# Optimization experiments

Hardware: AMD Instinct MI355X
Metric: run time of the kernel (lower is better)

## Reference

```python
import jax, jax.numpy as jnp
import numpy as np

N, D, K, STEPS, LAYERS, E = 20000, 128, 16, 2, 2, 8192


def setup_inputs() -> dict:
    key = jax.random.key(0)
    ks = jax.random.split(key, 8)
    return {
        "edges": jax.random.randint(ks[0], (E, 2), 0, N),
        "labels": jax.random.randint(ks[1], (E,), 0, 2).astype(jnp.int32),
        "neighbors": jax.random.randint(ks[2], (STEPS, N, K), 0, N),
        "embeddings": jax.random.normal(ks[3], (N, D), jnp.float32),
        "fc_w": jax.random.normal(ks[4], (2 * D,), jnp.float32) / np.sqrt(2.0 * D),
        "fc_b": jnp.zeros((), jnp.float32),
        "layer_w": jax.random.normal(ks[5], (LAYERS, D, D), jnp.float32) / np.sqrt(float(D)),
        "layer_b": jnp.zeros((LAYERS, D), jnp.float32),
    }


def _attention_all_nodes(embeddings, neighbors, fc_w, fc_b):
    # Vectorized GAT-style per-node attention over all N nodes, summed over steps.
    d = embeddings.shape[-1]
    w_n, w_s = fc_w[:d], fc_w[d:]  # fc applied to concat([neigh, self]) splits linearly
    out = jnp.zeros_like(embeddings)
    self_score = embeddings @ w_s  # [N]
    for s in range(neighbors.shape[0]):  # small fixed step count (2)
        nb = neighbors[s]                               # [N, K]
        neigh_emb = embeddings[nb]                      # [N, K, d]
        scores = neigh_emb @ w_n + self_score[:, None] + fc_b  # [N, K]
        scores = jnp.where(scores >= 0, scores, 0.2 * scores)  # LeakyReLU(0.2)
        attn = jax.nn.softmax(scores, axis=1)                  # softmax over neighbors
        k = nb.shape[1]
        # sum_k (neigh_emb * attn + self_emb) = weighted sum + K * self_emb
        agg = jnp.einsum("nkd,nk->nd", neigh_emb, attn) + k * embeddings
        out = out + agg
    return out


def reference(edges, labels, neighbors, embeddings, fc_w, fc_b, layer_w, layer_b):
    d = embeddings.shape[-1]
    att = _attention_all_nodes(embeddings, neighbors, fc_w, fc_b)  # [N, d]
    src, dst = edges[:, 0], edges[:, 1]
    use_att = (labels == 1)[:, None]
    src_e = jnp.where(use_att, att[src], embeddings[src])  # [E, d]
    dst_e = jnp.where(use_att, att[dst], embeddings[dst])  # [E, d]
    # layers applied in PARALLEL to the same input, relu'd, then summed
    src_l = jax.nn.relu(jnp.einsum("ed,lfd->led", src_e, layer_w) + layer_b[:, None, :])
    dst_l = jax.nn.relu(jnp.einsum("ed,lfd->led", dst_e, layer_w) + layer_b[:, None, :])
    src_sum = jnp.sum(src_l, axis=0)  # [E, d]
    dst_sum = jnp.sum(dst_l, axis=0)
    diff = jnp.sum((src_sum - dst_sum) ** 2, axis=1) / d  # [E]
    predicts = jnp.exp(-diff)
    loss = 0.5 * (labels.astype(predicts.dtype) - predicts) ** 2
    return jnp.sum(loss)
```

## Files before the change

### kernel.cpp

```cpp
#include <hip/hip_runtime.h>

#define N_NODES 20000
#define D 128
#define K 16
#define STEPS 2
#define E_EDGES 8192

#define SCORE_BLOCKS 2500
#define EDGE_BLOCKS 256
#define EDGE_WAVES (EDGE_BLOCKS * 8)


__device__ __forceinline__ unsigned short f2bf(float f) {
    unsigned u = __float_as_uint(f);
    u += 0x7FFFu + ((u >> 16) & 1u);
    return (unsigned short)(u >> 16);
}
__device__ __forceinline__ float bf2f(unsigned short h) {
    return __uint_as_float(((unsigned)h) << 16);
}

__global__ __launch_bounds__(256) void pre_kernel(
    const float* __restrict__ emb, const float* __restrict__ fc_w,
    const float* __restrict__ layer_w,
    unsigned short* __restrict__ emb_h, float* __restrict__ nscore,
    float* __restrict__ sscore, float* __restrict__ wsum,
    float* __restrict__ out)
{
    const int b = blockIdx.x;
    const int t = threadIdx.x;

    if (b < SCORE_BLOCKS) {
        const int wave = (b * 256 + t) >> 6;
        const int lane = t & 63;
        const int half = lane >> 5, sub = lane & 31;
        const int node = 2 * wave + half;

        const float4 e4  = *(const float4*)(emb + (size_t)node * D + sub * 4);
        const float4 wn4 = *(const float4*)(fc_w + sub * 4);
        const float4 ws4 = *(const float4*)(fc_w + D + sub * 4);
        float dn = e4.x * wn4.x + e4.y * wn4.y + e4.z * wn4.z + e4.w * wn4.w;
        float ds = e4.x * ws4.x + e4.y * ws4.y + e4.z * ws4.z + e4.w * ws4.w;
        #pragma unroll
        for (int off = 16; off > 0; off >>= 1) {
            dn += __shfl_xor(dn, off, 64);
            ds += __shfl_xor(ds, off, 64);
        }
        if (sub == 0) { nscore[node] = dn; sscore[node] = ds; }

        ushort4 h;
        h.x = f2bf(e4.x); h.y = f2bf(e4.y); h.z = f2bf(e4.z); h.w = f2bf(e4.w);
        *(ushort4*)(emb_h + (size_t)node * D + sub * 4) = h;
    } else {
        const int l = t >> 7, d = t & 127;
        const float* p = layer_w + (size_t)l * D * D + d;
        float s = 0.f;
        #pragma unroll
        for (int f = 0; f < D; f += 16) {
            float tmp[16];
            #pragma unroll
            for (int j = 0; j < 16; ++j) tmp[j] = p[(size_t)(f + j) * D];
            #pragma unroll
            for (int j = 0; j < 16; ++j) s += tmp[j];
        }
        wsum[t] = s;
        if (t == 0) out[0] = 0.f;
    }
}

__global__ __launch_bounds__(512) void edge_kernel(
    const int* __restrict__ edges, const int* __restrict__ labels,
    const int* __restrict__ neighbors, const float* __restrict__ emb,
    const unsigned short* __restrict__ emb_h,
    const float* __restrict__ nscore, const float* __restrict__ sscore,
    const float* __restrict__ fc_b, const float* __restrict__ wsum,
    const float* __restrict__ layer_b, float* __restrict__ out)
{
    __shared__ float part[8];
    const int t = threadIdx.x;
    const int lane = t & 63, wv = t >> 6;
    const int half = lane >> 5, sub = lane & 31;
    const int gw = blockIdx.x * 8 + wv;
    const float bias = fc_b[0];

    const float4 w0 = *(const float4*)(wsum + sub * 4);
    const float4 w1 = *(const float4*)(wsum + D + sub * 4);
    const float4 b0 = *(const float4*)(layer_b + sub * 4);
    const float4 b1 = *(const float4*)(layer_b + D + sub * 4);

    float local = 0.f;
    for (int e = gw; e < E_EDGES; e += EDGE_WAVES) {
        const int lab = labels[e];
        const int node = edges[2 * e + half];

        float4 x;
        if (lab == 1) {
            const int step = sub >> 4;
            const int idx = neighbors[((size_t)step * N_NODES + node) * K + (sub & 15)];
            const float raw = nscore[idx] + sscore[node] + bias;
            float sc = (raw >= 0.f) ? raw : 0.2f * raw;

            float m = sc;
            #pragma unroll
            for (int off = 8; off > 0; off >>= 1) m = fmaxf(m, __shfl_xor(m, off, 64));
            const float ex = __expf(sc - m);
            float den = ex;
            #pragma unroll
            for (int off = 8; off > 0; off >>= 1) den += __shfl_xor(den, off, 64);
            const float a = ex / den;

            const float4 e4 = *(const float4*)(emb + (size_t)node * D + sub * 4);
            x.x = (float)(STEPS * K) * e4.x;
            x.y = (float)(STEPS * K) * e4.y;
            x.z = (float)(STEPS * K) * e4.z;
            x.w = (float)(STEPS * K) * e4.w;
            const int base_lane = half << 5;
            #pragma unroll 8
            for (int k2 = 0; k2 < 32; ++k2) {
                const int   sl   = base_lane + k2;
                const int   idxk = __shfl(idx, sl, 64);
                const float ak   = __shfl(a, sl, 64);
                const ushort4 vh = *(const ushort4*)(emb_h + (size_t)idxk * D + sub * 4);
                x.x += ak * bf2f(vh.x);
                x.y += ak * bf2f(vh.y);
                x.z += ak * bf2f(vh.z);
                x.w += ak * bf2f(vh.w);
            }
        } else {
            x = *(const float4*)(emb + (size_t)node * D + sub * 4);
        }

        float4 ss;
        ss.x = fmaxf(x.x * w0.x + b0.x, 0.f) + fmaxf(x.x * w1.x + b1.x, 0.f);
        ss.y = fmaxf(x.y * w0.y + b0.y, 0.f) + fmaxf(x.y * w1.y + b1.y, 0.f);
        ss.z = fmaxf(x.z * w0.z + b0.z, 0.f) + fmaxf(x.z * w1.z + b1.z, 0.f);
        ss.w = fmaxf(x.w * w0.w + b0.w, 0.f) + fmaxf(x.w * w1.w + b1.w, 0.f);

        const float ox = __shfl_xor(ss.x, 32, 64);
        const float oy = __shfl_xor(ss.y, 32, 64);
        const float oz = __shfl_xor(ss.z, 32, 64);
        const float ow = __shfl_xor(ss.w, 32, 64);
        const float dx = ss.x - ox, dy = ss.y - oy, dz = ss.z - oz, dw = ss.w - ow;
        float v = dx * dx + dy * dy + dz * dz + dw * dw;
        #pragma unroll
        for (int off = 16; off > 0; off >>= 1) v += __shfl_xor(v, off, 64);

        const float pred = __expf(-(v * (1.0f / (float)D)));
        const float l = (float)lab - pred;
        local += 0.5f * l * l;
    }
    if (lane == 0) part[wv] = local;
    __syncthreads();
    if (t == 0) {
        float s = 0.f;
        #pragma unroll
        for (int i = 0; i < 8; ++i) s += part[i];
        atomicAdd(out, s);
    }
}

extern "C" void kernel_launch(void* const* d_in, const int* in_sizes, int n_in,
                              void* d_out, int out_size, void* d_ws, size_t ws_size,
                              hipStream_t stream) {
    const int*   edges     = (const int*)  d_in[0];
    const int*   labels    = (const int*)  d_in[1];
    const int*   neighbors = (const int*)  d_in[2];
    const float* emb       = (const float*)d_in[3];
    const float* fc_w      = (const float*)d_in[4];
    const float* fc_b      = (const float*)d_in[5];
    const float* layer_w   = (const float*)d_in[6];
    const float* layer_b   = (const float*)d_in[7];
    float* out = (float*)d_out;

    unsigned short* emb_h = (unsigned short*)d_ws;
    float* nscore = (float*)((char*)d_ws + (size_t)N_NODES * D * 2);
    float* sscore = nscore + N_NODES;
    float* wsum   = sscore + N_NODES;

    pre_kernel<<<SCORE_BLOCKS + 1, 256, 0, stream>>>(
        emb, fc_w, layer_w, emb_h, nscore, sscore, wsum, out);

    edge_kernel<<<EDGE_BLOCKS, 512, 0, stream>>>(
        edges, labels, neighbors, emb, emb_h, nscore, sscore,
        fc_b, wsum, layer_b, out);
}
```

Measured before the change: 95.48 us.

## Fuse preprocessing and edge kernels into one persistent kernel with grid barrier

Merges the node-score/bf16-conversion pre-pass and the edge loss pass into a single 256-block kernel. The two phases are separated by a software grid barrier built on global atomic counters and a generation number. This removes one kernel launch and the gap between launches. In exchange, it relies on all 256 blocks being co-resident, and the pre-pass now runs as a grid-stride loop over fewer waves. The emb row load is also hoisted so it is issued before the label branch.

Result: slower. 110.2 us (+15.4%).

```diff
diff --git a/kernel.cpp b/kernel.cpp
--- a/kernel.cpp
+++ b/kernel.cpp
@@ -6,10 +6,13 @@
 #define STEPS 2
 #define E_EDGES 8192
 
-#define SCORE_BLOCKS 2500
-#define EDGE_BLOCKS 256
-#define EDGE_WAVES (EDGE_BLOCKS * 8)
+#define GRID_BLOCKS 256
+#define TOTAL_WAVES (GRID_BLOCKS * 8)
+#define NODE_PAIRS (N_NODES / 2)
 
+
+__device__ unsigned g_cnt = 0u;
+__device__ unsigned g_gen = 0u;
 
 __device__ __forceinline__ unsigned short f2bf(float f) {
     unsigned u = __float_as_uint(f);
@@ -20,82 +23,92 @@
     return __uint_as_float(((unsigned)h) << 16);
 }
 
-__global__ __launch_bounds__(256) void pre_kernel(
-    const float* __restrict__ emb, const float* __restrict__ fc_w,
-    const float* __restrict__ layer_w,
+__global__ __launch_bounds__(512) void fused_kernel(
+    const int* __restrict__ edges, const int* __restrict__ labels,
+    const int* __restrict__ neighbors, const float* __restrict__ emb,
+    const float* __restrict__ fc_w, const float* __restrict__ fc_b,
+    const float* __restrict__ layer_w, const float* __restrict__ layer_b,
     unsigned short* __restrict__ emb_h, float* __restrict__ nscore,
     float* __restrict__ sscore, float* __restrict__ wsum,
     float* __restrict__ out)
 {
+    __shared__ float part[8];
+    const int t = threadIdx.x;
     const int b = blockIdx.x;
-    const int t = threadIdx.x;
+    const int lane = t & 63, wv = t >> 6;
+    const int half = lane >> 5, sub = lane & 31;
+    const int gw = b * 8 + wv;
 
-    if (b < SCORE_BLOCKS) {
-        const int wave = (b * 256 + t) >> 6;
-        const int lane = t & 63;
-        const int half = lane >> 5, sub = lane & 31;
-        const int node = 2 * wave + half;
+    const unsigned g0 = __hip_atomic_load(&g_gen, __ATOMIC_RELAXED, __HIP_MEMORY_SCOPE_AGENT);
 
-        const float4 e4  = *(const float4*)(emb + (size_t)node * D + sub * 4);
+    {
         const float4 wn4 = *(const float4*)(fc_w + sub * 4);
         const float4 ws4 = *(const float4*)(fc_w + D + sub * 4);
-        float dn = e4.x * wn4.x + e4.y * wn4.y + e4.z * wn4.z + e4.w * wn4.w;
-        float ds = e4.x * ws4.x + e4.y * ws4.y + e4.z * ws4.z + e4.w * ws4.w;
-        #pragma unroll
-        for (int off = 16; off > 0; off >>= 1) {
-            dn += __shfl_xor(dn, off, 64);
-            ds += __shfl_xor(ds, off, 64);
+        for (int p = gw; p < NODE_PAIRS; p += TOTAL_WAVES) {
+            const int node = 2 * p + half;
+            const float4 e4 = *(const float4*)(emb + (size_t)node * D + sub * 4);
+            float dn = e4.x * wn4.x + e4.y * wn4.y + e4.z * wn4.z + e4.w * wn4.w;
+            float ds = e4.x * ws4.x + e4.y * ws4.y + e4.z * ws4.z + e4.w * ws4.w;
+            #pragma unroll
+            for (int off = 16; off > 0; off >>= 1) {
+                dn += __shfl_xor(dn, off, 64);
+                ds += __shfl_xor(ds, off, 64);
+            }
+            if (sub == 0) { nscore[node] = dn; sscore[node] = ds; }
+            ushort4 h;
+            h.x = f2bf(e4.x); h.y = f2bf(e4.y); h.z = f2bf(e4.z); h.w = f2bf(e4.w);
+            *(ushort4*)(emb_h + (size_t)node * D + sub * 4) = h;
         }
-        if (sub == 0) { nscore[node] = dn; sscore[node] = ds; }
+        if (b == GRID_BLOCKS - 1 && t < 2 * D) {
+            const int l = t >> 7, d = t & 127;
+            const float* p = layer_w + (size_t)l * D * D + d;
+            float s = 0.f;
+            #pragma unroll
+            for (int f = 0; f < D; f += 16) {
+                float tmp[16];
+                #pragma unroll
+                for (int j = 0; j < 16; ++j) tmp[j] = p[(size_t)(f + j) * D];
+                #pragma unroll
+                for (int j = 0; j < 16; ++j) s += tmp[j];
+            }
+            wsum[t] = s;
+            if (t == 0) out[0] = 0.f;
+        }
+    }
 
-        ushort4 h;
-        h.x = f2bf(e4.x); h.y = f2bf(e4.y); h.z = f2bf(e4.z); h.w = f2bf(e4.w);
-        *(ushort4*)(emb_h + (size_t)node * D + sub * 4) = h;
-    } else {
-        const int l = t >> 7, d = t & 127;
-        const float* p = layer_w + (size_t)l * D * D + d;
-        float s = 0.f;
-        #pragma unroll
-        for (int f = 0; f < D; f += 16) {
-            float tmp[16];
-            #pragma unroll
-            for (int j = 0; j < 16; ++j) tmp[j] = p[(size_t)(f + j) * D];
-            #pragma unroll
-            for (int j = 0; j < 16; ++j) s += tmp[j];
+    __syncthreads();
+    if (t == 0) {
+        unsigned old = __hip_atomic_fetch_add(&g_cnt, 1u, __ATOMIC_ACQ_REL,
+                                              __HIP_MEMORY_SCOPE_AGENT);
+        if (old == GRID_BLOCKS - 1) {
+            __hip_atomic_fetch_add(&g_cnt, (unsigned)(0u - GRID_BLOCKS),
+                                   __ATOMIC_RELAXED, __HIP_MEMORY_SCOPE_AGENT);
+            __hip_atomic_fetch_add(&g_gen, 1u, __ATOMIC_ACQ_REL,
+                                   __HIP_MEMORY_SCOPE_AGENT);
+        } else {
+            while (__hip_atomic_fetch_add(&g_gen, 0u, __ATOMIC_RELAXED,
+                                          __HIP_MEMORY_SCOPE_AGENT) == g0) {
+                __builtin_amdgcn_s_sleep(1);
+            }
         }
-        wsum[t] = s;
-        if (t == 0) out[0] = 0.f;
+        (void)__hip_atomic_load(&g_gen, __ATOMIC_ACQUIRE, __HIP_MEMORY_SCOPE_AGENT);
     }
-}
+    __syncthreads();
 
-__global__ __launch_bounds__(512) void edge_kernel(
-    const int* __restrict__ edges, const int* __restrict__ labels,
-    const int* __restrict__ neighbors, const float* __restrict__ emb,
-    const unsigned short* __restrict__ emb_h,
-    const float* __restrict__ nscore, const float* __restrict__ sscore,
-    const float* __restrict__ fc_b, const float* __restrict__ wsum,
-    const float* __restrict__ layer_b, float* __restrict__ out)
-{
-    __shared__ float part[8];
-    const int t = threadIdx.x;
-    const int lane = t & 63, wv = t >> 6;
-    const int half = lane >> 5, sub = lane & 31;
-    const int gw = blockIdx.x * 8 + wv;
     const float bias = fc_b[0];
-
+    const int step = sub >> 4;
     const float4 w0 = *(const float4*)(wsum + sub * 4);
     const float4 w1 = *(const float4*)(wsum + D + sub * 4);
     const float4 b0 = *(const float4*)(layer_b + sub * 4);
     const float4 b1 = *(const float4*)(layer_b + D + sub * 4);
 
     float local = 0.f;
-    for (int e = gw; e < E_EDGES; e += EDGE_WAVES) {
+    for (int e = gw; e < E_EDGES; e += TOTAL_WAVES) {
         const int lab = labels[e];
         const int node = edges[2 * e + half];
 
-        float4 x;
+        float4 xx = *(const float4*)(emb + (size_t)node * D + sub * 4);
         if (lab == 1) {
-            const int step = sub >> 4;
             const int idx = neighbors[((size_t)step * N_NODES + node) * K + (sub & 15)];
             const float raw = nscore[idx] + sscore[node] + bias;
             float sc = (raw >= 0.f) ? raw : 0.2f * raw;
@@ -109,11 +122,8 @@
             for (int off = 8; off > 0; off >>= 1) den += __shfl_xor(den, off, 64);
             const float a = ex / den;
 
-            const float4 e4 = *(const float4*)(emb + (size_t)node * D + sub * 4);
-            x.x = (float)(STEPS * K) * e4.x;
-            x.y = (float)(STEPS * K) * e4.y;
-            x.z = (float)(STEPS * K) * e4.z;
-            x.w = (float)(STEPS * K) * e4.w;
+            xx.x *= (float)(STEPS * K); xx.y *= (float)(STEPS * K);
+            xx.z *= (float)(STEPS * K); xx.w *= (float)(STEPS * K);
             const int base_lane = half << 5;
             #pragma unroll 8
             for (int k2 = 0; k2 < 32; ++k2) {
@@ -121,20 +131,18 @@
                 const int   idxk = __shfl(idx, sl, 64);
                 const float ak   = __shfl(a, sl, 64);
                 const ushort4 vh = *(const ushort4*)(emb_h + (size_t)idxk * D + sub * 4);
-                x.x += ak * bf2f(vh.x);
-                x.y += ak * bf2f(vh.y);
-                x.z += ak * bf2f(vh.z);
-                x.w += ak * bf2f(vh.w);
+                xx.x += ak * bf2f(vh.x);
+                xx.y += ak * bf2f(vh.y);
+                xx.z += ak * bf2f(vh.z);
+                xx.w += ak * bf2f(vh.w);
             }
-        } else {
-            x = *(const float4*)(emb + (size_t)node * D + sub * 4);
         }
 
         float4 ss;
-        ss.x = fmaxf(x.x * w0.x + b0.x, 0.f) + fmaxf(x.x * w1.x + b1.x, 0.f);
-        ss.y = fmaxf(x.y * w0.y + b0.y, 0.f) + fmaxf(x.y * w1.y + b1.y, 0.f);
-        ss.z = fmaxf(x.z * w0.z + b0.z, 0.f) + fmaxf(x.z * w1.z + b1.z, 0.f);
-        ss.w = fmaxf(x.w * w0.w + b0.w, 0.f) + fmaxf(x.w * w1.w + b1.w, 0.f);
+        ss.x = fmaxf(xx.x * w0.x + b0.x, 0.f) + fmaxf(xx.x * w1.x + b1.x, 0.f);
+        ss.y = fmaxf(xx.y * w0.y + b0.y, 0.f) + fmaxf(xx.y * w1.y + b1.y, 0.f);
+        ss.z = fmaxf(xx.z * w0.z + b0.z, 0.f) + fmaxf(xx.z * w1.z + b1.z, 0.f);
+        ss.w = fmaxf(xx.w * w0.w + b0.w, 0.f) + fmaxf(xx.w * w1.w + b1.w, 0.f);
 
         const float ox = __shfl_xor(ss.x, 32, 64);
         const float oy = __shfl_xor(ss.y, 32, 64);
@@ -149,6 +157,7 @@
         const float l = (float)lab - pred;
         local += 0.5f * l * l;
     }
+
     if (lane == 0) part[wv] = local;
     __syncthreads();
     if (t == 0) {
@@ -177,10 +186,7 @@
     float* sscore = nscore + N_NODES;
     float* wsum   = sscore + N_NODES;
 
-    pre_kernel<<<SCORE_BLOCKS + 1, 256, 0, stream>>>(
-        emb, fc_w, layer_w, emb_h, nscore, sscore, wsum, out);
-
-    edge_kernel<<<EDGE_BLOCKS, 512, 0, stream>>>(
-        edges, labels, neighbors, emb, emb_h, nscore, sscore,
-        fc_b, wsum, layer_b, out);
+    fused_kernel<<<GRID_BLOCKS, 512, 0, stream>>>(
+        edges, labels, neighbors, emb, fc_w, fc_b, layer_w, layer_b,
+        emb_h, nscore, sscore, wsum, out);
 }
```
